# Kernel optimization log

Hardware: AMD Instinct MI355X
Metric: run time of the kernel (lower is better)

## Reference

```python
import jax, jax.numpy as jnp
import numpy as np

D_EMB = 1024
D_MODEL = 1024
NUM_ROLES = 4
ROLE_DIM = 64
ROPE_BASE = 10000.0
LN_EPS = 1e-5


def _rope_cos_sin(positions):
    # positions: [B, S] float -> cos, sin: [B, S, D_MODEL//2]
    inv_freq = 1.0 / (ROPE_BASE ** (jnp.arange(0, D_MODEL, 2, dtype=jnp.float32) / D_MODEL))
    freqs = positions[..., None] * inv_freq  # [B,S,d/2]
    return jnp.cos(freqs), jnp.sin(freqs)


def _apply_rotary(x, cos, sin):
    d = x.shape[-1] // 2
    x1, x2 = x[..., :d], x[..., d:]
    return jnp.concatenate([x1 * cos - x2 * sin, x1 * sin + x2 * cos], axis=-1)


def _layernorm(x, g, b):
    mu = jnp.mean(x, axis=-1, keepdims=True)
    var = jnp.var(x, axis=-1, keepdims=True)
    return (x - mu) * jax.lax.rsqrt(var + LN_EPS) * g + b


def setup_inputs() -> dict:
    key = jax.random.key(0)
    ks = jax.random.split(key, 16)
    B, S, M = 16, 4096, 200
    inp = {}
    inp["x_ctx"] = jax.random.normal(ks[0], (B, M, D_EMB), dtype=jnp.float32)
    inp["x_suf"] = jax.random.normal(ks[1], (B, S, D_EMB), dtype=jnp.float32)
    inp["pos_ctx"] = jax.random.randint(ks[2], (B, M), 0, 8192, dtype=jnp.int32)
    inp["pos_suf"] = jnp.sort(jax.random.randint(ks[3], (B, S), 0, 8192, dtype=jnp.int32), axis=-1)
    inp["role_ctx"] = jax.random.randint(ks[4], (B, M), 0, NUM_ROLES, dtype=jnp.int32)
    inp["role_tgt"] = jax.random.randint(ks[5], (B,), 0, NUM_ROLES, dtype=jnp.int32)
    inp["mask_ctx"] = jax.random.randint(ks[6], (B, M), 0, 2, dtype=jnp.int32)
    inp["mask_suf"] = jax.random.randint(ks[7], (B, S), 0, 2, dtype=jnp.int32)
    # parameters
    inp["ln_g"] = jnp.ones((D_EMB,), jnp.float32)
    inp["ln_b"] = jnp.zeros((D_EMB,), jnp.float32)
    inp["hist_role_emb"] = jax.random.normal(ks[8], (NUM_ROLES, ROLE_DIM), dtype=jnp.float32)
    inp["tgt_role_emb"] = jax.random.normal(ks[9], (NUM_ROLES, ROLE_DIM), dtype=jnp.float32)
    inp["start_state"] = jax.random.normal(ks[10], (D_EMB + ROLE_DIM,), dtype=jnp.float32) * 0.02
    inp["wq"] = jax.random.normal(ks[11], (D_MODEL, D_EMB + 2 * ROLE_DIM), dtype=jnp.float32) * 0.02
    inp["wk"] = jax.random.normal(ks[12], (D_MODEL, D_EMB), dtype=jnp.float32) * 0.02
    inp["u_w1"] = jax.random.normal(ks[13], (D_MODEL, D_EMB), dtype=jnp.float32) * 0.02
    inp["u_b1"] = jnp.zeros((D_MODEL,), jnp.float32)
    inp["u_w2"] = jax.random.normal(ks[14], (NUM_ROLES, D_MODEL), dtype=jnp.float32) * 0.02
    inp["u_b2"] = jnp.zeros((NUM_ROLES,), jnp.float32)
    return inp


def reference(x_ctx, x_suf, pos_ctx, pos_suf, role_ctx, role_tgt, mask_ctx, mask_suf,
              ln_g, ln_b, hist_role_emb, tgt_role_emb, start_state,
              wq, wk, u_w1, u_b1, u_w2, u_b2):
    B, S, _ = x_suf.shape
    scale = 1.0 / jnp.sqrt(jnp.asarray(D_MODEL, jnp.float32))

    # ---- history summary: last valid token's features + its role embedding ----
    lengths = jnp.sum(mask_ctx.astype(jnp.int32), axis=1)          # [B]
    last_idx = jnp.clip(lengths - 1, 0, None)                       # [B]
    last_x = jnp.take_along_axis(x_ctx, last_idx[:, None, None], axis=1)[:, 0]  # [B, d_emb]
    last_role = jnp.take_along_axis(role_ctx, last_idx[:, None], axis=1)[:, 0]  # [B]
    cand = jnp.concatenate([last_x, hist_role_emb[last_role]], axis=-1)  # [B, d_emb+role_dim]
    summary = jnp.where((lengths > 0)[:, None], cand, start_state[None, :])

    # ---- query / keys ----
    q_in = jnp.concatenate([summary, tgt_role_emb[role_tgt]], axis=-1)  # [B, d_emb+2*role_dim]
    x_s = _layernorm(x_suf, ln_g, ln_b)                                 # [B, S, d_emb]

    anchor = pos_suf[:, :1].astype(jnp.float32) - 1.0                   # [B, 1]
    q_cos, q_sin = _rope_cos_sin(anchor)                                # [B, 1, d/2]
    k_cos, k_sin = _rope_cos_sin(pos_suf.astype(jnp.float32))           # [B, S, d/2]

    q = (q_in @ wq.T)[:, None, :]                                       # [B, 1, d_model]
    k = jnp.einsum('bse,de->bsd', x_s, wk)                              # [B, S, d_model]
    q = _apply_rotary(q, q_cos, q_sin)
    k = _apply_rotary(k, k_cos, k_sin)

    logits = jnp.einsum('bd,bsd->bs', q[:, 0], k) * scale               # [B, S]

    # ---- unary logits, gathered at target role ----
    h = jax.nn.gelu(jnp.einsum('bse,de->bsd', x_s, u_w1) + u_b1, approximate=False)
    unary_all = jnp.einsum('bsd,rd->bsr', h, u_w2) + u_b2               # [B, S, num_roles]
    unary = jnp.take_along_axis(unary_all, role_tgt[:, None, None].astype(jnp.int32), axis=-1)[..., 0]
    logits = logits + unary

    logits = jnp.where(mask_suf == 0, -jnp.inf, logits)
    return logits, jnp.argmax(logits, axis=-1)
```

## Files before the change

### kernel.cpp

```cpp
#include <hip/hip_runtime.h>
#include <math.h>

#define B_SZ 16
#define S_LEN 4096
#define M_CTX 200
#define DE 1024
#define NTOK (B_SZ * S_LEN)

#define MASK_SENTINEL -3.0e38f

typedef __attribute__((ext_vector_type(8))) short short8v;
typedef __attribute__((ext_vector_type(4))) float f32x4;

__device__ __forceinline__ unsigned short f2bf(float f) {
  unsigned x = __float_as_uint(f);
  unsigned r = x + 0x7fffu + ((x >> 16) & 1u);
  return (unsigned short)(r >> 16);
}
__device__ __forceinline__ float bf2f(unsigned short u) {
  return __uint_as_float(((unsigned)u) << 16);
}
__device__ __forceinline__ void gload16(const unsigned short* g, short* l) {
  __builtin_amdgcn_global_load_lds(
      (const __attribute__((address_space(1))) unsigned int*)g,
      (__attribute__((address_space(3))) unsigned int*)l, 16, 0, 0);
}

__global__ __launch_bounds__(256) void invf_kernel(float* __restrict__ invf_g) {
  int i = blockIdx.x * 256 + threadIdx.x;
  invf_g[i] = 1.0f / powf(10000.0f, (float)(2 * i) * (1.0f / 1024.0f));
}

__global__ __launch_bounds__(256) void prep_qin_kernel(
    const float* __restrict__ x_ctx, const int* __restrict__ role_ctx,
    const int* __restrict__ role_tgt, const int* __restrict__ mask_ctx,
    const float* __restrict__ hist_role_emb, const float* __restrict__ tgt_role_emb,
    const float* __restrict__ start_state, float* __restrict__ qin_ws)
{
  int b = blockIdx.x;
  int tid = threadIdx.x;
  __shared__ int sh[3];
  if (tid == 0) {
    int len = 0;
    for (int m = 0; m < M_CTX; ++m) len += (mask_ctx[b * M_CTX + m] != 0) ? 1 : 0;
    int li = len - 1; if (li < 0) li = 0;
    sh[0] = len; sh[1] = li; sh[2] = role_ctx[b * M_CTX + li];
  }
  __syncthreads();
  int len = sh[0], li = sh[1], lrole = sh[2];
  int rt = role_tgt[b];
  for (int e = tid; e < 1152; e += 256) {
    float v;
    if (e < 1024)      v = (len > 0) ? x_ctx[((size_t)b * M_CTX + li) * DE + e] : start_state[e];
    else if (e < 1088) v = (len > 0) ? hist_role_emb[lrole * 64 + (e - 1024)] : start_state[e];
    else               v = tgt_role_emb[rt * 64 + (e - 1088)];
    qin_ws[b * 1152 + e] = v;
  }
}

__global__ __launch_bounds__(256) void matvec_q_kernel(
    const float* __restrict__ qin_ws, const float* __restrict__ wq,
    float* __restrict__ qv_ws)
{
  int dblk = blockIdx.x, b = blockIdx.y;
  int tid = threadIdx.x, lane = tid & 63, w = tid >> 6;
  __shared__ float q[1152];
  for (int i = tid; i < 1152; i += 256) q[i] = qin_ws[b * 1152 + i];
  __syncthreads();
  #pragma unroll 4
  for (int i = 0; i < 16; ++i) {
    int d = dblk * 64 + w * 16 + i;
    const float* wr = wq + (size_t)d * 1152;
    float s = 0.f;
    #pragma unroll
    for (int j = 0; j < 18; ++j) s += q[j * 64 + lane] * wr[j * 64 + lane];
    #pragma unroll
    for (int off = 32; off; off >>= 1) s += __shfl_down(s, off);
    if (lane == 0) qv_ws[b * 1024 + d] = s;
  }
}

__global__ __launch_bounds__(256) void rot_q_kernel(
    const float* __restrict__ qv_ws, const float* __restrict__ invf_g,
    const int* __restrict__ pos_suf, float* __restrict__ q_rot)
{
  int b = blockIdx.x;
  int tid = threadIdx.x;
  float anchor = (float)pos_suf[(size_t)b * S_LEN] - 1.0f;
  const float scl = 1.0f / 32.0f;
  for (int i = tid; i < 512; i += 256) {
    float sn, cs;
    sincosf(anchor * invf_g[i], &sn, &cs);
    float q1 = qv_ws[b * 1024 + i], q2 = qv_ws[b * 1024 + i + 512];
    q_rot[b * 1024 + i]       = (q1 * cs - q2 * sn) * scl;
    q_rot[b * 1024 + i + 512] = (q1 * sn + q2 * cs) * scl;
  }
}

__global__ __launch_bounds__(256) void split_A_kernel(
    const float* __restrict__ x_suf, const float* __restrict__ ln_g,
    const float* __restrict__ ln_b,
    unsigned short* __restrict__ Ah, unsigned short* __restrict__ Al)
{
  int wave = threadIdx.x >> 6;
  int lane = threadIdx.x & 63;
  size_t t = (size_t)blockIdx.x * 4 + wave;
  const float4* xp = (const float4*)(x_suf + t * DE);
  float4 v[4];
  float s = 0.f, sq = 0.f;
  #pragma unroll
  for (int i = 0; i < 4; ++i) {
    v[i] = xp[lane + 64 * i];
    s  += v[i].x + v[i].y + v[i].z + v[i].w;
    sq += v[i].x * v[i].x + v[i].y * v[i].y + v[i].z * v[i].z + v[i].w * v[i].w;
  }
  #pragma unroll
  for (int off = 32; off; off >>= 1) {
    s  += __shfl_down(s, off);
    sq += __shfl_down(sq, off);
  }
  s = __shfl(s, 0); sq = __shfl(sq, 0);
  float m = s * (1.0f / 1024.0f);
  float rs = rsqrtf(sq * (1.0f / 1024.0f) - m * m + 1e-5f);
  #pragma unroll
  for (int i = 0; i < 4; ++i) {
    int e0 = (lane + 64 * i) * 4;
    float4 gv = *(const float4*)&ln_g[e0];
    float4 bv = *(const float4*)&ln_b[e0];
    float a0 = (v[i].x - m) * rs * gv.x + bv.x;
    float a1 = (v[i].y - m) * rs * gv.y + bv.y;
    float a2 = (v[i].z - m) * rs * gv.z + bv.z;
    float a3 = (v[i].w - m) * rs * gv.w + bv.w;
    ushort4 hi, lo;
    hi.x = f2bf(a0); lo.x = f2bf(a0 - bf2f(hi.x));
    hi.y = f2bf(a1); lo.y = f2bf(a1 - bf2f(hi.y));
    hi.z = f2bf(a2); lo.z = f2bf(a2 - bf2f(hi.z));
    hi.w = f2bf(a3); lo.w = f2bf(a3 - bf2f(hi.w));
    *(ushort4*)&Ah[t * DE + e0] = hi;
    *(ushort4*)&Al[t * DE + e0] = lo;
  }
}

__global__ __launch_bounds__(256) void split_B_kernel(
    const float* __restrict__ wk, const float* __restrict__ u_w1,
    unsigned short* __restrict__ Bh, unsigned short* __restrict__ Bl)
{
  size_t i4 = (size_t)blockIdx.x * 256 + threadIdx.x;
  size_t e0 = i4 * 4;
  size_t row = e0 >> 10;
  size_t off = e0 & 1023;
  const float* src = (row < 1024) ? (wk + row * 1024 + off)
                                  : (u_w1 + (row - 1024) * 1024 + off);
  float4 v = *(const float4*)src;
  ushort4 hi, lo;
  hi.x = f2bf(v.x); lo.x = f2bf(v.x - bf2f(hi.x));
  hi.y = f2bf(v.y); lo.y = f2bf(v.y - bf2f(hi.y));
  hi.z = f2bf(v.z); lo.z = f2bf(v.z - bf2f(hi.z));
  hi.w = f2bf(v.w); lo.w = f2bf(v.w - bf2f(hi.w));
  *(ushort4*)&Bh[e0] = hi;
  *(ushort4*)&Bl[e0] = lo;
}

__global__ __launch_bounds__(256, 2) void mfma_gemm_kernel(
    const unsigned short* __restrict__ Ah, const unsigned short* __restrict__ Al,
    const unsigned short* __restrict__ Bh, const unsigned short* __restrict__ Bl,
    unsigned short* __restrict__ kb, unsigned short* __restrict__ hb)
{
  __shared__ __align__(16) short lAh[128 * 32];
  __shared__ __align__(16) short lAl[128 * 32];
  __shared__ __align__(16) short lBh[128 * 32];
  __shared__ __align__(16) short lBl[128 * 32];

  int lin = blockIdx.y * 16 + blockIdx.x;
  int swz = (lin & 7) * 1024 + (lin >> 3);
  int nt = swz & 15;
  size_t gt0 = (size_t)(swz >> 4) * 128;
  int tid = threadIdx.x;
  int lane = tid & 63;
  int wid = tid >> 6;
  int wr = wid >> 1, wc = wid & 1;
  size_t n0 = (size_t)nt * 128;

  const unsigned short* gsrc; short* ldst; size_t rbase;
  if (wid == 0)      { gsrc = Ah; ldst = lAh; rbase = gt0; }
  else if (wid == 1) { gsrc = Al; ldst = lAl; rbase = gt0; }
  else if (wid == 2) { gsrc = Bh; ldst = lBh; rbase = n0; }
  else               { gsrc = Bl; ldst = lBl; rbase = n0; }

  f32x4 acc[4][4];
  #pragma unroll
  for (int i = 0; i < 4; ++i)
    #pragma unroll
    for (int j = 0; j < 4; ++j) acc[i][j] = (f32x4)0.f;

  for (int kk = 0; kk < 1024; kk += 32) {
    #pragma unroll
    for (int it = 0; it < 8; ++it) {
      int row = it * 16 + (lane >> 2);
      int g = (lane & 3) ^ ((row >> 1) & 3);
      gload16(gsrc + (rbase + row) * 1024 + kk + g * 8, ldst + it * 512);
    }
    __syncthreads();

    short8v a_h[4], a_l[4], b_h[4], b_l[4];
    #pragma unroll
    for (int f = 0; f < 4; ++f) {
      int r = wr * 64 + f * 16 + (lane & 15);
      int idx = r * 32 + (((lane >> 4) ^ ((r >> 1) & 3)) << 3);
      a_h[f] = *(const short8v*)&lAh[idx];
      a_l[f] = *(const short8v*)&lAl[idx];
      int c = wc * 64 + f * 16 + (lane & 15);
      int idxb = c * 32 + (((lane >> 4) ^ ((c >> 1) & 3)) << 3);
      b_h[f] = *(const short8v*)&lBh[idxb];
      b_l[f] = *(const short8v*)&lBl[idxb];
    }

    #define MFMA_(ACC, A, B) \
      asm volatile("v_mfma_f32_16x16x32_bf16 %0, %1, %2, %0" : "+v"(ACC) : "v"(A), "v"(B))
    #pragma unroll
    for (int i = 0; i < 4; ++i)
      #pragma unroll
      for (int j = 0; j < 4; ++j) MFMA_(acc[i][j], a_h[i], b_h[j]);
    #pragma unroll
    for (int i = 0; i < 4; ++i)
      #pragma unroll
      for (int j = 0; j < 4; ++j) MFMA_(acc[i][j], a_h[i], b_l[j]);
    #pragma unroll
    for (int i = 0; i < 4; ++i)
      #pragma unroll
      for (int j = 0; j < 4; ++j) MFMA_(acc[i][j], a_l[i], b_h[j]);
    #undef MFMA_
    __syncthreads();
  }

  asm volatile("s_nop 7\n\ts_nop 7\n\ts_nop 7");

  unsigned short* outb = (nt < 8) ? kb : hb;
  size_t ncol0 = (nt < 8) ? n0 : n0 - 1024;
  #pragma unroll
  for (int fi = 0; fi < 4; ++fi)
    #pragma unroll
    for (int fj = 0; fj < 4; ++fj) {
      size_t col = ncol0 + wc * 64 + fj * 16 + (lane & 15);
      #pragma unroll
      for (int r = 0; r < 4; ++r) {
        size_t t = gt0 + wr * 64 + fi * 16 + (lane >> 4) * 4 + r;
        outb[t * 1024 + col] = f2bf(acc[fi][fj][r]);
      }
    }
}

__global__ __launch_bounds__(256) void ep_kernel(
    const unsigned short* __restrict__ kb, const unsigned short* __restrict__ hb,
    const float* __restrict__ q_rot, const float* __restrict__ invf_g,
    const int* __restrict__ pos_suf, const int* __restrict__ role_tgt,
    const float* __restrict__ u_b1, const float* __restrict__ u_w2,
    const float* __restrict__ u_b2, const int* __restrict__ mask_suf,
    float* __restrict__ out)
{
  __shared__ float sInv[512];
  for (int i = threadIdx.x; i < 512; i += 256) sInv[i] = invf_g[i];
  __syncthreads();

  int wave = threadIdx.x >> 6;
  int lane = threadIdx.x & 63;
  size_t t = (size_t)blockIdx.x * 4 + wave;
  int b = (int)(t >> 12);
  int role = role_tgt[b];
  float pos = (float)pos_suf[t];
  float s = 0.f;

  {
    int c0 = lane * 8;
    short8v k1 = *(const short8v*)&kb[t * 1024 + c0];
    short8v k2 = *(const short8v*)&kb[t * 1024 + 512 + c0];
    float4 q1a = *(const float4*)&q_rot[b * 1024 + c0];
    float4 q1b = *(const float4*)&q_rot[b * 1024 + c0 + 4];
    float4 q2a = *(const float4*)&q_rot[b * 1024 + 512 + c0];
    float4 q2b = *(const float4*)&q_rot[b * 1024 + 512 + c0 + 4];
    float q1v[8] = {q1a.x, q1a.y, q1a.z, q1a.w, q1b.x, q1b.y, q1b.z, q1b.w};
    float q2v[8] = {q2a.x, q2a.y, q2a.z, q2a.w, q2b.x, q2b.y, q2b.z, q2b.w};
    #pragma unroll
    for (int j = 0; j < 8; ++j) {
      float sn, cs;
      sincosf(pos * sInv[c0 + j], &sn, &cs);
      s += bf2f((unsigned short)k1[j]) * (q1v[j] * cs + q2v[j] * sn)
         + bf2f((unsigned short)k2[j]) * (q2v[j] * cs - q1v[j] * sn);
    }
  }
  {
    int c0 = lane * 16;
    short8v h1 = *(const short8v*)&hb[t * 1024 + c0];
    short8v h2 = *(const short8v*)&hb[t * 1024 + c0 + 8];
    #pragma unroll
    for (int half = 0; half < 2; ++half) {
      short8v hv = half ? h2 : h1;
      int cc = c0 + half * 8;
      float4 b1a = *(const float4*)&u_b1[cc];
      float4 b1b = *(const float4*)&u_b1[cc + 4];
      float4 w2a = *(const float4*)&u_w2[role * 1024 + cc];
      float4 w2b = *(const float4*)&u_w2[role * 1024 + cc + 4];
      float b1v[8] = {b1a.x, b1a.y, b1a.z, b1a.w, b1b.x, b1b.y, b1b.z, b1b.w};
      float w2v[8] = {w2a.x, w2a.y, w2a.z, w2a.w, w2b.x, w2b.y, w2b.z, w2b.w};
      #pragma unroll
      for (int j = 0; j < 8; ++j) {
        float pre = bf2f((unsigned short)hv[j]) + b1v[j];
        float g = pre * 0.5f * (1.0f + erff(pre * 0.70710678118f));
        s += g * w2v[j];
      }
    }
  }
  #pragma unroll
  for (int off = 32; off; off >>= 1) s += __shfl_down(s, off);
  if (lane == 0) {
    float v = s + u_b2[role];
    if (mask_suf[t] == 0) v = MASK_SENTINEL;
    out[t] = v;
  }
}

__global__ __launch_bounds__(256) void argmax_kernel(
    const float* __restrict__ logits, float* __restrict__ out)
{
  int b = blockIdx.x;
  int tid = threadIdx.x;
  float bestv = -INFINITY;
  int besti = 0x7fffffff;
  for (int s = tid; s < S_LEN; s += 256) {
    float v = logits[(size_t)b * S_LEN + s];
    if (v > bestv || (v == bestv && s < besti)) { bestv = v; besti = s; }
  }
  __shared__ float sv[256];
  __shared__ int si[256];
  sv[tid] = bestv; si[tid] = besti;
  __syncthreads();
  for (int off = 128; off; off >>= 1) {
    if (tid < off) {
      float ov = sv[tid + off]; int oi = si[tid + off];
      if (ov > sv[tid] || (ov == sv[tid] && oi < si[tid])) { sv[tid] = ov; si[tid] = oi; }
    }
    __syncthreads();
  }
  if (tid == 0) out[(size_t)B_SZ * S_LEN + b] = (float)si[0];
}

__global__ __launch_bounds__(256) void ln_stats_kernel(
    const float* __restrict__ x_suf, float* __restrict__ mu, float* __restrict__ rstd)
{
  int wave = threadIdx.x >> 6;
  int lane = threadIdx.x & 63;
  size_t t = (size_t)blockIdx.x * 4 + wave;
  const float4* xp = (const float4*)(x_suf + t * DE);
  float s = 0.f, sq = 0.f;
  #pragma unroll
  for (int i = 0; i < 4; ++i) {
    float4 v = xp[lane + 64 * i];
    s  += v.x + v.y + v.z + v.w;
    sq += v.x * v.x + v.y * v.y + v.z * v.z + v.w * v.w;
  }
  #pragma unroll
  for (int off = 32; off; off >>= 1) {
    s  += __shfl_down(s, off);
    sq += __shfl_down(sq, off);
  }
  if (lane == 0) {
    float m = s * (1.0f / 1024.0f);
    float var = sq * (1.0f / 1024.0f) - m * m;
    mu[t] = m;
    rstd[t] = rsqrtf(var + 1e-5f);
  }
}

#define BM 128
#define BN 128
#define BKF 32
#define LDP 132

__global__ __launch_bounds__(256) void main_gemm_kernel(
    const float* __restrict__ x_suf, const float* __restrict__ wk,
    const float* __restrict__ u_w1, const float* __restrict__ ln_g,
    const float* __restrict__ ln_b, const float* __restrict__ mu,
    const float* __restrict__ rstd, const float* __restrict__ q_rot,
    const int* __restrict__ pos_suf, const int* __restrict__ role_tgt,
    const float* __restrict__ u_b1, const float* __restrict__ u_w2,
    float* __restrict__ accb)
{
  __shared__ float As[BKF][LDP];
  __shared__ float Bs[BKF][LDP];
  __shared__ float sInvf[512];

  int nt = blockIdx.x;
  size_t tt = blockIdx.y;
  int tid = threadIdx.x;
  size_t gt0 = tt * BM;
  int b = (int)(gt0 >> 12);

  for (int i = tid; i < 512; i += 256)
    sInvf[i] = 1.0f / powf(10000.0f, (float)(2 * i) * (1.0f / 1024.0f));

  int lr = tid >> 3;
  int lc = (tid & 7) * 4;
  float lmu[4], lrs[4];
  #pragma unroll
  for (int r = 0; r < 4; ++r) {
    lmu[r] = mu[gt0 + lr + 32 * r];
    lrs[r] = rstd[gt0 + lr + 32 * r];
  }
  const float* Wb = (nt < 8) ? wk : u_w1;
  int rowoff = (nt < 8) ? nt * BN : nt * BN - 1024;

  float acc[8][8];
  #pragma unroll
  for (int i = 0; i < 8; ++i)
    #pragma unroll
    for (int j = 0; j < 8; ++j) acc[i][j] = 0.f;

  int tx = tid & 15, ty = tid >> 4;

  for (int kk = 0; kk < 1024; kk += BKF) {
    float4 gv = *(const float4*)&ln_g[kk + lc];
    float4 bv = *(const float4*)&ln_b[kk + lc];
    #pragma unroll
    for (int r = 0; r < 4; ++r) {
      int row = lr + 32 * r;
      float4 xv = *(const float4*)&x_suf[(gt0 + row) * (size_t)DE + kk + lc];
      float m = lmu[r], rs = lrs[r];
      As[lc + 0][row] = (xv.x - m) * rs * gv.x + bv.x;
      As[lc + 1][row] = (xv.y - m) * rs * gv.y + bv.y;
      As[lc + 2][row] = (xv.z - m) * rs * gv.z + bv.z;
      As[lc + 3][row] = (xv.w - m) * rs * gv.w + bv.w;
      float4 wv = *(const float4*)&Wb[(size_t)(rowoff + row) * 1024 + kk + lc];
      Bs[lc + 0][row] = wv.x;
      Bs[lc + 1][row] = wv.y;
      Bs[lc + 2][row] = wv.z;
      Bs[lc + 3][row] = wv.w;
    }
    __syncthreads();
    #pragma unroll 8
    for (int k = 0; k < BKF; ++k) {
      float a[8], bb[8];
      *(float4*)&a[0]  = *(const float4*)&As[k][ty * 8];
      *(float4*)&a[4]  = *(const float4*)&As[k][ty * 8 + 4];
      *(float4*)&bb[0] = *(const float4*)&Bs[k][tx * 8];
      *(float4*)&bb[4] = *(const float4*)&Bs[k][tx * 8 + 4];
      #pragma unroll
      for (int i = 0; i < 8; ++i)
        #pragma unroll
        for (int j = 0; j < 8; ++j)
          acc[i][j] += a[i] * bb[j];
    }
    __syncthreads();
  }

  int role = role_tgt[b];
  float part[8];
  int cb = nt * BN + tx * 8;
  if (nt < 8) {
    #pragma unroll
    for (int i = 0; i < 8; ++i) {
      size_t t = gt0 + ty * 8 + i;
      float pos = (float)pos_suf[t];
      float p = 0.f;
      #pragma unroll
      for (int j = 0; j < 8; ++j) {
        int c = cb + j;
        int ii = (c < 512) ? c : (c - 512);
        float sn, cs;
        sincosf(pos * sInvf[ii], &sn, &cs);
        float q1 = q_rot[b * 1024 + ii];
        float q2 = q_rot[b * 1024 + ii + 512];
        float qe = (c < 512) ? (q1 * cs + q2 * sn) : (q2 * cs - q1 * sn);
        p += acc[i][j] * qe;
      }
      part[i] = p;
    }
  } else {
    #pragma unroll
    for (int i = 0; i < 8; ++i) {
      float p = 0.f;
      #pragma unroll
      for (int j = 0; j < 8; ++j) {
        int c = cb - 1024 + j;
        float pre = acc[i][j] + u_b1[c];
        float h = pre * 0.5f * (1.0f + erff(pre * 0.70710678118f));
        p += h * u_w2[role * 1024 + c];
      }
      part[i] = p;
    }
  }
  #pragma unroll
  for (int off = 8; off >= 1; off >>= 1) {
    #pragma unroll
    for (int i = 0; i < 8; ++i) part[i] += __shfl_down(part[i], off, 16);
  }
  if (tx == 0) {
    #pragma unroll
    for (int i = 0; i < 8; ++i) atomicAdd(&accb[gt0 + ty * 8 + i], part[i]);
  }
}

__global__ __launch_bounds__(256) void finalize_kernel(
    const float* __restrict__ accb, const int* __restrict__ mask_suf,
    const int* __restrict__ role_tgt, const float* __restrict__ u_b2,
    float* __restrict__ out)
{
  int b = blockIdx.x;
  int tid = threadIdx.x;
  float ub = u_b2[role_tgt[b]];
  float bestv = -INFINITY;
  int besti = 0x7fffffff;
  for (int s = tid; s < S_LEN; s += 256) {
    float v = accb[(size_t)b * S_LEN + s] + ub;
    if (mask_suf[(size_t)b * S_LEN + s] == 0) v = MASK_SENTINEL;
    out[(size_t)b * S_LEN + s] = v;
    if (v > bestv || (v == bestv && s < besti)) { bestv = v; besti = s; }
  }
  __shared__ float sv[256];
  __shared__ int si[256];
  sv[tid] = bestv; si[tid] = besti;
  __syncthreads();
  for (int off = 128; off; off >>= 1) {
    if (tid < off) {
      float ov = sv[tid + off]; int oi = si[tid + off];
      if (ov > sv[tid] || (ov == sv[tid] && oi < si[tid])) { sv[tid] = ov; si[tid] = oi; }
    }
    __syncthreads();
  }
  if (tid == 0) out[(size_t)B_SZ * S_LEN + b] = (float)si[0];
}

extern "C" void kernel_launch(void* const* d_in, const int* in_sizes, int n_in,
                              void* d_out, int out_size, void* d_ws, size_t ws_size,
                              hipStream_t stream)
{
  const float* x_ctx         = (const float*)d_in[0];
  const float* x_suf         = (const float*)d_in[1];
  const int*   pos_suf       = (const int*)d_in[3];
  const int*   role_ctx      = (const int*)d_in[4];
  const int*   role_tgt      = (const int*)d_in[5];
  const int*   mask_ctx      = (const int*)d_in[6];
  const int*   mask_suf      = (const int*)d_in[7];
  const float* ln_g          = (const float*)d_in[8];
  const float* ln_b          = (const float*)d_in[9];
  const float* hist_role_emb = (const float*)d_in[10];
  const float* tgt_role_emb  = (const float*)d_in[11];
  const float* start_state   = (const float*)d_in[12];
  const float* wq            = (const float*)d_in[13];
  const float* wk            = (const float*)d_in[14];
  const float* u_w1          = (const float*)d_in[15];
  const float* u_b1          = (const float*)d_in[16];
  const float* u_w2          = (const float*)d_in[17];
  const float* u_b2          = (const float*)d_in[18];
  float* out = (float*)d_out;
  char* ws = (char*)d_ws;

  const size_t OFF_QROT = 0;
  const size_t OFF_INVF = 65536;
  const size_t OFF_QIN  = OFF_INVF + 4096;
  const size_t OFF_QV   = OFF_QIN + 81920;
  const size_t OFF_BH   = 1 << 20;
  const size_t OFF_BL   = OFF_BH + 4194304;
  const size_t OFF_AH   = OFF_BL + 4194304;
  const size_t OFF_AL   = OFF_AH + 134217728;
  const size_t OFF_KB   = OFF_AL + 134217728;
  const size_t OFF_HB   = OFF_KB + 134217728;
  const size_t NEEDED   = OFF_HB + 134217728;

  if (ws_size >= NEEDED) {
    float* q_rot = (float*)(ws + OFF_QROT);
    float* invf_g = (float*)(ws + OFF_INVF);
    float* qin_ws = (float*)(ws + OFF_QIN);
    float* qv_ws  = (float*)(ws + OFF_QV);
    unsigned short* Bh = (unsigned short*)(ws + OFF_BH);
    unsigned short* Bl = (unsigned short*)(ws + OFF_BL);
    unsigned short* Ah = (unsigned short*)(ws + OFF_AH);
    unsigned short* Al = (unsigned short*)(ws + OFF_AL);
    unsigned short* kb = (unsigned short*)(ws + OFF_KB);
    unsigned short* hb = (unsigned short*)(ws + OFF_HB);

    invf_kernel<<<2, 256, 0, stream>>>(invf_g);
    prep_qin_kernel<<<B_SZ, 256, 0, stream>>>(
        x_ctx, role_ctx, role_tgt, mask_ctx,
        hist_role_emb, tgt_role_emb, start_state, qin_ws);
    matvec_q_kernel<<<dim3(16, B_SZ), 256, 0, stream>>>(qin_ws, wq, qv_ws);
    rot_q_kernel<<<B_SZ, 256, 0, stream>>>(qv_ws, invf_g, pos_suf, q_rot);
    split_B_kernel<<<2048, 256, 0, stream>>>(wk, u_w1, Bh, Bl);
    split_A_kernel<<<NTOK / 4, 256, 0, stream>>>(x_suf, ln_g, ln_b, Ah, Al);
    dim3 gg(16, NTOK / 128);
    mfma_gemm_kernel<<<gg, 256, 0, stream>>>(Ah, Al, Bh, Bl, kb, hb);
    ep_kernel<<<NTOK / 4, 256, 0, stream>>>(
        kb, hb, q_rot, invf_g, pos_suf, role_tgt, u_b1, u_w2, u_b2, mask_suf, out);
    argmax_kernel<<<B_SZ, 256, 0, stream>>>(out, out);
  } else {
    float* q_rot = (float*)ws;
    float* mu    = (float*)(ws + (64 << 10));
    float* rstd  = (float*)(ws + (64 << 10) + (256 << 10));
    float* accb  = (float*)(ws + (64 << 10) + (512 << 10));

    hipMemsetAsync(accb, 0, NTOK * sizeof(float), stream);
    prep_qin_kernel<<<B_SZ, 256, 0, stream>>>(
        x_ctx, role_ctx, role_tgt, mask_ctx,
        hist_role_emb, tgt_role_emb, start_state, q_rot);
    matvec_q_kernel<<<dim3(16, B_SZ), 256, 0, stream>>>(q_rot, wq, rstd);
    rot_q_kernel<<<B_SZ, 256, 0, stream>>>(rstd, mu, pos_suf, q_rot);
    ln_stats_kernel<<<NTOK / 4, 256, 0, stream>>>(x_suf, mu, rstd);
    dim3 g3(16, NTOK / BM);
    main_gemm_kernel<<<g3, 256, 0, stream>>>(
        x_suf, wk, u_w1, ln_g, ln_b, mu, rstd, q_rot,
        pos_suf, role_tgt, u_b1, u_w2, accb);
    finalize_kernel<<<B_SZ, 256, 0, stream>>>(accb, mask_suf, role_tgt, u_b2, out);
  }
}
```

Baseline: 1.288 ms.

## Fuse RoPE/GELU epilogue into MFMA GEMM with atomic row reduction

The GEMM epilogue now applies the rotary dot product with q, or GELU with the u_w2 projection, directly on the accumulators. It reduces across the 16 lanes of a row and atomically adds per-token partial sums into a float buffer. The two 128MB bf16 intermediates (kb, hb) and the separate epilogue kernel are removed, and argmax is merged with the mask/bias finalize step. The block swizzle is dropped for a plain grid mapping, which may hurt L2 reuse. The fused epilogue also adds sincos/erf work and atomics inside the GEMM, and atomic ordering makes the sums nondeterministic.

```diff
diff --git a/kernel.cpp b/kernel.cpp
--- a/kernel.cpp
+++ b/kernel.cpp
@@ -161,25 +161,47 @@
   *(ushort4*)&Bl[e0] = lo;
 }
 
-__global__ __launch_bounds__(256, 2) void mfma_gemm_kernel(
+__global__ __launch_bounds__(256, 2) void mfma_gemm_fused_kernel(
     const unsigned short* __restrict__ Ah, const unsigned short* __restrict__ Al,
     const unsigned short* __restrict__ Bh, const unsigned short* __restrict__ Bl,
-    unsigned short* __restrict__ kb, unsigned short* __restrict__ hb)
+    const float* __restrict__ q_rot, const float* __restrict__ invf_g,
+    const int* __restrict__ pos_suf, const int* __restrict__ role_tgt,
+    const float* __restrict__ u_b1, const float* __restrict__ u_w2,
+    float* __restrict__ accb)
 {
   __shared__ __align__(16) short lAh[128 * 32];
   __shared__ __align__(16) short lAl[128 * 32];
   __shared__ __align__(16) short lBh[128 * 32];
   __shared__ __align__(16) short lBl[128 * 32];
-
-  int lin = blockIdx.y * 16 + blockIdx.x;
-  int swz = (lin & 7) * 1024 + (lin >> 3);
-  int nt = swz & 15;
-  size_t gt0 = (size_t)(swz >> 4) * 128;
+  __shared__ float sPos[128];
+  __shared__ float sC0[128];
+  __shared__ float sC1[128];
+  __shared__ float sC2[128];
+
+  int nt = blockIdx.x;
+  size_t gt0 = (size_t)blockIdx.y * 128;
+  int b = (int)(gt0 >> 12);
   int tid = threadIdx.x;
   int lane = tid & 63;
   int wid = tid >> 6;
   int wr = wid >> 1, wc = wid & 1;
   size_t n0 = (size_t)nt * 128;
+
+  if (tid < 128) {
+    int j = tid;
+    sPos[j] = (float)pos_suf[gt0 + j];
+    if (nt < 8) {
+      int c = nt * 128 + j;
+      int ii = c & 511;
+      sC0[j] = q_rot[b * 1024 + ii];
+      sC1[j] = q_rot[b * 1024 + ii + 512];
+      sC2[j] = invf_g[ii];
+    } else {
+      int cc = nt * 128 - 1024 + j;
+      sC0[j] = u_b1[cc];
+      sC1[j] = u_w2[role_tgt[b] * 1024 + cc];
+    }
+  }
 
   const unsigned short* gsrc; short* ldst; size_t rbase;
   if (wid == 0)      { gsrc = Ah; ldst = lAh; rbase = gt0; }
@@ -235,99 +257,76 @@
 
   asm volatile("s_nop 7\n\ts_nop 7\n\ts_nop 7");
 
-  unsigned short* outb = (nt < 8) ? kb : hb;
-  size_t ncol0 = (nt < 8) ? n0 : n0 - 1024;
+  float vsum[4][4];
+  if (nt < 8) {
+    bool lowhalf = (nt < 4);
+    #pragma unroll
+    for (int fi = 0; fi < 4; ++fi)
+      #pragma unroll
+      for (int r = 0; r < 4; ++r) {
+        int row = wr * 64 + fi * 16 + ((lane >> 4) << 2) + r;
+        float p = sPos[row];
+        float vs = 0.f;
+        #pragma unroll
+        for (int fj = 0; fj < 4; ++fj) {
+          int j = wc * 64 + fj * 16 + (lane & 15);
+          float sn, cs;
+          sincosf(p * sC2[j], &sn, &cs);
+          float qe = lowhalf ? (sC0[j] * cs + sC1[j] * sn)
+                             : (sC1[j] * cs - sC0[j] * sn);
+          vs += acc[fi][fj][r] * qe;
+        }
+        vsum[fi][r] = vs;
+      }
+  } else {
+    #pragma unroll
+    for (int fi = 0; fi < 4; ++fi)
+      #pragma unroll
+      for (int r = 0; r < 4; ++r) {
+        float vs = 0.f;
+        #pragma unroll
+        for (int fj = 0; fj < 4; ++fj) {
+          int j = wc * 64 + fj * 16 + (lane & 15);
+          float pre = acc[fi][fj][r] + sC0[j];
+          float g = pre * 0.5f * (1.0f + erff(pre * 0.70710678118f));
+          vs += g * sC1[j];
+        }
+        vsum[fi][r] = vs;
+      }
+  }
   #pragma unroll
   for (int fi = 0; fi < 4; ++fi)
     #pragma unroll
-    for (int fj = 0; fj < 4; ++fj) {
-      size_t col = ncol0 + wc * 64 + fj * 16 + (lane & 15);
+    for (int r = 0; r < 4; ++r) {
+      #pragma unroll
+      for (int off = 1; off < 16; off <<= 1)
+        vsum[fi][r] += __shfl_xor(vsum[fi][r], off, 16);
+    }
+  if ((lane & 15) == 0) {
+    #pragma unroll
+    for (int fi = 0; fi < 4; ++fi)
       #pragma unroll
       for (int r = 0; r < 4; ++r) {
-        size_t t = gt0 + wr * 64 + fi * 16 + (lane >> 4) * 4 + r;
-        outb[t * 1024 + col] = f2bf(acc[fi][fj][r]);
+        size_t t = gt0 + wr * 64 + fi * 16 + ((lane >> 4) << 2) + r;
+        atomicAdd(&accb[t], vsum[fi][r]);
       }
-    }
-}
-
-__global__ __launch_bounds__(256) void ep_kernel(
-    const unsigned short* __restrict__ kb, const unsigned short* __restrict__ hb,
-    const float* __restrict__ q_rot, const float* __restrict__ invf_g,
-    const int* __restrict__ pos_suf, const int* __restrict__ role_tgt,
-    const float* __restrict__ u_b1, const float* __restrict__ u_w2,
-    const float* __restrict__ u_b2, const int* __restrict__ mask_suf,
+  }
+}
+
+__global__ __launch_bounds__(256) void finalize_kernel(
+    const float* __restrict__ accb, const int* __restrict__ mask_suf,
+    const int* __restrict__ role_tgt, const float* __restrict__ u_b2,
     float* __restrict__ out)
-{
-  __shared__ float sInv[512];
-  for (int i = threadIdx.x; i < 512; i += 256) sInv[i] = invf_g[i];
-  __syncthreads();
-
-  int wave = threadIdx.x >> 6;
-  int lane = threadIdx.x & 63;
-  size_t t = (size_t)blockIdx.x * 4 + wave;
-  int b = (int)(t >> 12);
-  int role = role_tgt[b];
-  float pos = (float)pos_suf[t];
-  float s = 0.f;
-
-  {
-    int c0 = lane * 8;
-    short8v k1 = *(const short8v*)&kb[t * 1024 + c0];
-    short8v k2 = *(const short8v*)&kb[t * 1024 + 512 + c0];
-    float4 q1a = *(const float4*)&q_rot[b * 1024 + c0];
-    float4 q1b = *(const float4*)&q_rot[b * 1024 + c0 + 4];
-    float4 q2a = *(const float4*)&q_rot[b * 1024 + 512 + c0];
-    float4 q2b = *(const float4*)&q_rot[b * 1024 + 512 + c0 + 4];
-    float q1v[8] = {q1a.x, q1a.y, q1a.z, q1a.w, q1b.x, q1b.y, q1b.z, q1b.w};
-    float q2v[8] = {q2a.x, q2a.y, q2a.z, q2a.w, q2b.x, q2b.y, q2b.z, q2b.w};
-    #pragma unroll
-    for (int j = 0; j < 8; ++j) {
-      float sn, cs;
-      sincosf(pos * sInv[c0 + j], &sn, &cs);
-      s += bf2f((unsigned short)k1[j]) * (q1v[j] * cs + q2v[j] * sn)
-         + bf2f((unsigned short)k2[j]) * (q2v[j] * cs - q1v[j] * sn);
-    }
-  }
-  {
-    int c0 = lane * 16;
-    short8v h1 = *(const short8v*)&hb[t * 1024 + c0];
-    short8v h2 = *(const short8v*)&hb[t * 1024 + c0 + 8];
-    #pragma unroll
-    for (int half = 0; half < 2; ++half) {
-      short8v hv = half ? h2 : h1;
-      int cc = c0 + half * 8;
-      float4 b1a = *(const float4*)&u_b1[cc];
-      float4 b1b = *(const float4*)&u_b1[cc + 4];
-      float4 w2a = *(const float4*)&u_w2[role * 1024 + cc];
-      float4 w2b = *(const float4*)&u_w2[role * 1024 + cc + 4];
-      float b1v[8] = {b1a.x, b1a.y, b1a.z, b1a.w, b1b.x, b1b.y, b1b.z, b1b.w};
-      float w2v[8] = {w2a.x, w2a.y, w2a.z, w2a.w, w2b.x, w2b.y, w2b.z, w2b.w};
-      #pragma unroll
-      for (int j = 0; j < 8; ++j) {
-        float pre = bf2f((unsigned short)hv[j]) + b1v[j];
-        float g = pre * 0.5f * (1.0f + erff(pre * 0.70710678118f));
-        s += g * w2v[j];
-      }
-    }
-  }
-  #pragma unroll
-  for (int off = 32; off; off >>= 1) s += __shfl_down(s, off);
-  if (lane == 0) {
-    float v = s + u_b2[role];
-    if (mask_suf[t] == 0) v = MASK_SENTINEL;
-    out[t] = v;
-  }
-}
-
-__global__ __launch_bounds__(256) void argmax_kernel(
-    const float* __restrict__ logits, float* __restrict__ out)
 {
   int b = blockIdx.x;
   int tid = threadIdx.x;
+  float ub = u_b2[role_tgt[b]];
   float bestv = -INFINITY;
   int besti = 0x7fffffff;
   for (int s = tid; s < S_LEN; s += 256) {
-    float v = logits[(size_t)b * S_LEN + s];
+    float v = accb[(size_t)b * S_LEN + s] + ub;
+    if (mask_suf[(size_t)b * S_LEN + s] == 0) v = MASK_SENTINEL;
+    out[(size_t)b * S_LEN + s] = v;
     if (v > bestv || (v == bestv && s < besti)) { bestv = v; besti = s; }
   }
   __shared__ float sv[256];
@@ -497,36 +496,6 @@
     #pragma unroll
     for (int i = 0; i < 8; ++i) atomicAdd(&accb[gt0 + ty * 8 + i], part[i]);
   }
-}
-
-__global__ __launch_bounds__(256) void finalize_kernel(
-    const float* __restrict__ accb, const int* __restrict__ mask_suf,
-    const int* __restrict__ role_tgt, const float* __restrict__ u_b2,
-    float* __restrict__ out)
-{
-  int b = blockIdx.x;
-  int tid = threadIdx.x;
-  float ub = u_b2[role_tgt[b]];
-  float bestv = -INFINITY;
-  int besti = 0x7fffffff;
-  for (int s = tid; s < S_LEN; s += 256) {
-    float v = accb[(size_t)b * S_LEN + s] + ub;
-    if (mask_suf[(size_t)b * S_LEN + s] == 0) v = MASK_SENTINEL;
-    out[(size_t)b * S_LEN + s] = v;
-    if (v > bestv || (v == bestv && s < besti)) { bestv = v; besti = s; }
-  }
-  __shared__ float sv[256];
-  __shared__ int si[256];
-  sv[tid] = bestv; si[tid] = besti;
-  __syncthreads();
-  for (int off = 128; off; off >>= 1) {
-    if (tid < off) {
-      float ov = sv[tid + off]; int oi = si[tid + off];
-      if (ov > sv[tid] || (ov == sv[tid] && oi < si[tid])) { sv[tid] = ov; si[tid] = oi; }
-    }
-    __syncthreads();
-  }
-  if (tid == 0) out[(size_t)B_SZ * S_LEN + b] = (float)si[0];
 }
 
 extern "C" void kernel_launch(void* const* d_in, const int* in_sizes, int n_in,
@@ -558,26 +527,25 @@
   const size_t OFF_INVF = 65536;
   const size_t OFF_QIN  = OFF_INVF + 4096;
   const size_t OFF_QV   = OFF_QIN + 81920;
+  const size_t OFF_ACCB = OFF_QV + 65536;
   const size_t OFF_BH   = 1 << 20;
   const size_t OFF_BL   = OFF_BH + 4194304;
   const size_t OFF_AH   = OFF_BL + 4194304;
   const size_t OFF_AL   = OFF_AH + 134217728;
-  const size_t OFF_KB   = OFF_AL + 134217728;
-  const size_t OFF_HB   = OFF_KB + 134217728;
-  const size_t NEEDED   = OFF_HB + 134217728;
+  const size_t NEEDED   = OFF_AL + 134217728;
 
   if (ws_size >= NEEDED) {
-    float* q_rot = (float*)(ws + OFF_QROT);
+    float* q_rot  = (float*)(ws + OFF_QROT);
     float* invf_g = (float*)(ws + OFF_INVF);
     float* qin_ws = (float*)(ws + OFF_QIN);
     float* qv_ws  = (float*)(ws + OFF_QV);
+    float* accb   = (float*)(ws + OFF_ACCB);
     unsigned short* Bh = (unsigned short*)(ws + OFF_BH);
     unsigned short* Bl = (unsigned short*)(ws + OFF_BL);
     unsigned short* Ah = (unsigned short*)(ws + OFF_AH);
     unsigned short* Al = (unsigned short*)(ws + OFF_AL);
-    unsigned short* kb = (unsigned short*)(ws + OFF_KB);
-    unsigned short* hb = (unsigned short*)(ws + OFF_HB);
-
+
+    hipMemsetAsync(accb, 0, NTOK * sizeof(float), stream);
     invf_kernel<<<2, 256, 0, stream>>>(invf_g);
     prep_qin_kernel<<<B_SZ, 256, 0, stream>>>(
         x_ctx, role_ctx, role_tgt, mask_ctx,
@@ -587,22 +555,25 @@
     split_B_kernel<<<2048, 256, 0, stream>>>(wk, u_w1, Bh, Bl);
     split_A_kernel<<<NTOK / 4, 256, 0, stream>>>(x_suf, ln_g, ln_b, Ah, Al);
     dim3 gg(16, NTOK / 128);
-    mfma_gemm_kernel<<<gg, 256, 0, stream>>>(Ah, Al, Bh, Bl, kb, hb);
-    ep_kernel<<<NTOK / 4, 256, 0, stream>>>(
-        kb, hb, q_rot, invf_g, pos_suf, role_tgt, u_b1, u_w2, u_b2, mask_suf, out);
-    argmax_kernel<<<B_SZ, 256, 0, stream>>>(out, out);
+    mfma_gemm_fused_kernel<<<gg, 256, 0, stream>>>(
+        Ah, Al, Bh, Bl, q_rot, invf_g, pos_suf, role_tgt, u_b1, u_w2, accb);
+    finalize_kernel<<<B_SZ, 256, 0, stream>>>(accb, mask_suf, role_tgt, u_b2, out);
   } else {
-    float* q_rot = (float*)ws;
-    float* mu    = (float*)(ws + (64 << 10));
-    float* rstd  = (float*)(ws + (64 << 10) + (256 << 10));
-    float* accb  = (float*)(ws + (64 << 10) + (512 << 10));
+    float* q_rot  = (float*)ws;
+    float* mu     = (float*)(ws + (64 << 10));
+    float* rstd   = (float*)(ws + (320 << 10));
+    float* accb   = (float*)(ws + (576 << 10));
+    float* qin_ws = (float*)(ws + (832 << 10));
+    float* qv_ws  = (float*)(ws + (912 << 10));
+    float* invf_g = (float*)(ws + (976 << 10));
 
     hipMemsetAsync(accb, 0, NTOK * sizeof(float), stream);
+    invf_kernel<<<2, 256, 0, stream>>>(invf_g);
     prep_qin_kernel<<<B_SZ, 256, 0, stream>>>(
         x_ctx, role_ctx, role_tgt, mask_ctx,
-        hist_role_emb, tgt_role_emb, start_state, q_rot);
-    matvec_q_kernel<<<dim3(16, B_SZ), 256, 0, stream>>>(q_rot, wq, rstd);
-    rot_q_kernel<<<B_SZ, 256, 0, stream>>>(rstd, mu, pos_suf, q_rot);
+        hist_role_emb, tgt_role_emb, start_state, qin_ws);
+    matvec_q_kernel<<<dim3(16, B_SZ), 256, 0, stream>>>(qin_ws, wq, qv_ws);
+    rot_q_kernel<<<B_SZ, 256, 0, stream>>>(qv_ws, invf_g, pos_suf, q_rot);
     ln_stats_kernel<<<NTOK / 4, 256, 0, stream>>>(x_suf, mu, rstd);
     dim3 g3(16, NTOK / BM);
     main_gemm_kernel<<<g3, 256, 0, stream>>>(
```

New measurement: 4.291 ms. +233.2%, slower.

## Precompute RoPE cos/sin lookup table and simplify epilogue and GEMM tile mapping

Applied to the files above, without the earlier changes.

Adds a kernel that builds per-position cos/sin tables for all 8192 possible positions, so the epilogue reads them instead of calling sincosf per element. The epilogue loads are reorganised to strided per-lane scalar accesses, and the GEMM drops its block-index swizzle in favour of a direct mapping. The fallback path's workspace layout is also fixed so it stops aliasing buffers. The table costs 32 MB of writes plus gather reads per token, and removing the swizzle may hurt L2 reuse in the GEMM.

```diff
diff --git a/kernel.cpp b/kernel.cpp
--- a/kernel.cpp
+++ b/kernel.cpp
@@ -6,6 +6,7 @@
 #define M_CTX 200
 #define DE 1024
 #define NTOK (B_SZ * S_LEN)
+#define POS_MAX 8192
 
 #define MASK_SENTINEL -3.0e38f
 
@@ -29,6 +30,20 @@
 __global__ __launch_bounds__(256) void invf_kernel(float* __restrict__ invf_g) {
   int i = blockIdx.x * 256 + threadIdx.x;
   invf_g[i] = 1.0f / powf(10000.0f, (float)(2 * i) * (1.0f / 1024.0f));
+}
+
+__global__ __launch_bounds__(256) void lut_kernel(
+    const float* __restrict__ invf_g,
+    float* __restrict__ lutc, float* __restrict__ luts)
+{
+  int p = blockIdx.x;
+  float fp = (float)p;
+  for (int c = threadIdx.x; c < 512; c += 256) {
+    float sn, cs;
+    sincosf(fp * invf_g[c], &sn, &cs);
+    lutc[(size_t)p * 512 + c] = cs;
+    luts[(size_t)p * 512 + c] = sn;
+  }
 }
 
 __global__ __launch_bounds__(256) void prep_qin_kernel(
@@ -171,10 +186,8 @@
   __shared__ __align__(16) short lBh[128 * 32];
   __shared__ __align__(16) short lBl[128 * 32];
 
-  int lin = blockIdx.y * 16 + blockIdx.x;
-  int swz = (lin & 7) * 1024 + (lin >> 3);
-  int nt = swz & 15;
-  size_t gt0 = (size_t)(swz >> 4) * 128;
+  int nt = blockIdx.x;
+  size_t gt0 = (size_t)blockIdx.y * 128;
   int tid = threadIdx.x;
   int lane = tid & 63;
   int wid = tid >> 6;
@@ -252,63 +265,41 @@
 
 __global__ __launch_bounds__(256) void ep_kernel(
     const unsigned short* __restrict__ kb, const unsigned short* __restrict__ hb,
-    const float* __restrict__ q_rot, const float* __restrict__ invf_g,
-    const int* __restrict__ pos_suf, const int* __restrict__ role_tgt,
-    const float* __restrict__ u_b1, const float* __restrict__ u_w2,
-    const float* __restrict__ u_b2, const int* __restrict__ mask_suf,
-    float* __restrict__ out)
-{
-  __shared__ float sInv[512];
-  for (int i = threadIdx.x; i < 512; i += 256) sInv[i] = invf_g[i];
-  __syncthreads();
-
+    const float* __restrict__ q_rot, const float* __restrict__ lutc,
+    const float* __restrict__ luts, const int* __restrict__ pos_suf,
+    const int* __restrict__ role_tgt, const float* __restrict__ u_b1,
+    const float* __restrict__ u_w2, const float* __restrict__ u_b2,
+    const int* __restrict__ mask_suf, float* __restrict__ out)
+{
   int wave = threadIdx.x >> 6;
   int lane = threadIdx.x & 63;
   size_t t = (size_t)blockIdx.x * 4 + wave;
   int b = (int)(t >> 12);
   int role = role_tgt[b];
-  float pos = (float)pos_suf[t];
+  size_t lbase = (size_t)pos_suf[t] * 512;
+  const unsigned short* kp = kb + t * 1024;
+  const unsigned short* hp = hb + t * 1024;
+  const float* lc = lutc + lbase;
+  const float* ls = luts + lbase;
+  const float* qr = q_rot + b * 1024;
+  const float* w2 = u_w2 + role * 1024;
   float s = 0.f;
 
-  {
-    int c0 = lane * 8;
-    short8v k1 = *(const short8v*)&kb[t * 1024 + c0];
-    short8v k2 = *(const short8v*)&kb[t * 1024 + 512 + c0];
-    float4 q1a = *(const float4*)&q_rot[b * 1024 + c0];
-    float4 q1b = *(const float4*)&q_rot[b * 1024 + c0 + 4];
-    float4 q2a = *(const float4*)&q_rot[b * 1024 + 512 + c0];
-    float4 q2b = *(const float4*)&q_rot[b * 1024 + 512 + c0 + 4];
-    float q1v[8] = {q1a.x, q1a.y, q1a.z, q1a.w, q1b.x, q1b.y, q1b.z, q1b.w};
-    float q2v[8] = {q2a.x, q2a.y, q2a.z, q2a.w, q2b.x, q2b.y, q2b.z, q2b.w};
-    #pragma unroll
-    for (int j = 0; j < 8; ++j) {
-      float sn, cs;
-      sincosf(pos * sInv[c0 + j], &sn, &cs);
-      s += bf2f((unsigned short)k1[j]) * (q1v[j] * cs + q2v[j] * sn)
-         + bf2f((unsigned short)k2[j]) * (q2v[j] * cs - q1v[j] * sn);
-    }
-  }
-  {
-    int c0 = lane * 16;
-    short8v h1 = *(const short8v*)&hb[t * 1024 + c0];
-    short8v h2 = *(const short8v*)&hb[t * 1024 + c0 + 8];
-    #pragma unroll
-    for (int half = 0; half < 2; ++half) {
-      short8v hv = half ? h2 : h1;
-      int cc = c0 + half * 8;
-      float4 b1a = *(const float4*)&u_b1[cc];
-      float4 b1b = *(const float4*)&u_b1[cc + 4];
-      float4 w2a = *(const float4*)&u_w2[role * 1024 + cc];
-      float4 w2b = *(const float4*)&u_w2[role * 1024 + cc + 4];
-      float b1v[8] = {b1a.x, b1a.y, b1a.z, b1a.w, b1b.x, b1b.y, b1b.z, b1b.w};
-      float w2v[8] = {w2a.x, w2a.y, w2a.z, w2a.w, w2b.x, w2b.y, w2b.z, w2b.w};
-      #pragma unroll
-      for (int j = 0; j < 8; ++j) {
-        float pre = bf2f((unsigned short)hv[j]) + b1v[j];
-        float g = pre * 0.5f * (1.0f + erff(pre * 0.70710678118f));
-        s += g * w2v[j];
-      }
-    }
+  #pragma unroll
+  for (int j = 0; j < 8; ++j) {
+    int c = lane + 64 * j;
+    float k1 = bf2f(kp[c]);
+    float k2 = bf2f(kp[c + 512]);
+    float q1 = qr[c], q2 = qr[c + 512];
+    float cs = lc[c], sn = ls[c];
+    s += k1 * (q1 * cs + q2 * sn) + k2 * (q2 * cs - q1 * sn);
+  }
+  #pragma unroll
+  for (int j = 0; j < 16; ++j) {
+    int c = lane + 64 * j;
+    float pre = bf2f(hp[c]) + u_b1[c];
+    float g = pre * 0.5f * (1.0f + erff(pre * 0.70710678118f));
+    s += g * w2[c];
   }
   #pragma unroll
   for (int off = 32; off; off >>= 1) s += __shfl_down(s, off);
@@ -556,21 +547,25 @@
 
   const size_t OFF_QROT = 0;
   const size_t OFF_INVF = 65536;
-  const size_t OFF_QIN  = OFF_INVF + 4096;
-  const size_t OFF_QV   = OFF_QIN + 81920;
+  const size_t OFF_QIN  = 69632;
+  const size_t OFF_QV   = 151552;
   const size_t OFF_BH   = 1 << 20;
   const size_t OFF_BL   = OFF_BH + 4194304;
-  const size_t OFF_AH   = OFF_BL + 4194304;
+  const size_t OFF_LUTC = OFF_BL + 4194304;
+  const size_t OFF_LUTS = OFF_LUTC + 16777216;
+  const size_t OFF_AH   = OFF_LUTS + 16777216;
   const size_t OFF_AL   = OFF_AH + 134217728;
   const size_t OFF_KB   = OFF_AL + 134217728;
   const size_t OFF_HB   = OFF_KB + 134217728;
   const size_t NEEDED   = OFF_HB + 134217728;
 
   if (ws_size >= NEEDED) {
-    float* q_rot = (float*)(ws + OFF_QROT);
+    float* q_rot  = (float*)(ws + OFF_QROT);
     float* invf_g = (float*)(ws + OFF_INVF);
     float* qin_ws = (float*)(ws + OFF_QIN);
     float* qv_ws  = (float*)(ws + OFF_QV);
+    float* lutc   = (float*)(ws + OFF_LUTC);
+    float* luts   = (float*)(ws + OFF_LUTS);
     unsigned short* Bh = (unsigned short*)(ws + OFF_BH);
     unsigned short* Bl = (unsigned short*)(ws + OFF_BL);
     unsigned short* Ah = (unsigned short*)(ws + OFF_AH);
@@ -579,6 +574,7 @@
     unsigned short* hb = (unsigned short*)(ws + OFF_HB);
 
     invf_kernel<<<2, 256, 0, stream>>>(invf_g);
+    lut_kernel<<<POS_MAX, 256, 0, stream>>>(invf_g, lutc, luts);
     prep_qin_kernel<<<B_SZ, 256, 0, stream>>>(
         x_ctx, role_ctx, role_tgt, mask_ctx,
         hist_role_emb, tgt_role_emb, start_state, qin_ws);
@@ -589,20 +585,25 @@
     dim3 gg(16, NTOK / 128);
     mfma_gemm_kernel<<<gg, 256, 0, stream>>>(Ah, Al, Bh, Bl, kb, hb);
     ep_kernel<<<NTOK / 4, 256, 0, stream>>>(
-        kb, hb, q_rot, invf_g, pos_suf, role_tgt, u_b1, u_w2, u_b2, mask_suf, out);
+        kb, hb, q_rot, lutc, luts, pos_suf, role_tgt, u_b1, u_w2, u_b2,
+        mask_suf, out);
     argmax_kernel<<<B_SZ, 256, 0, stream>>>(out, out);
   } else {
-    float* q_rot = (float*)ws;
-    float* mu    = (float*)(ws + (64 << 10));
-    float* rstd  = (float*)(ws + (64 << 10) + (256 << 10));
-    float* accb  = (float*)(ws + (64 << 10) + (512 << 10));
+    float* q_rot  = (float*)ws;
+    float* mu     = (float*)(ws + (64 << 10));
+    float* rstd   = (float*)(ws + (320 << 10));
+    float* accb   = (float*)(ws + (576 << 10));
+    float* qin_ws = (float*)(ws + (832 << 10));
+    float* qv_ws  = (float*)(ws + (912 << 10));
+    float* invf_g = (float*)(ws + (976 << 10));
 
     hipMemsetAsync(accb, 0, NTOK * sizeof(float), stream);
+    invf_kernel<<<2, 256, 0, stream>>>(invf_g);
     prep_qin_kernel<<<B_SZ, 256, 0, stream>>>(
         x_ctx, role_ctx, role_tgt, mask_ctx,
-        hist_role_emb, tgt_role_emb, start_state, q_rot);
-    matvec_q_kernel<<<dim3(16, B_SZ), 256, 0, stream>>>(q_rot, wq, rstd);
-    rot_q_kernel<<<B_SZ, 256, 0, stream>>>(rstd, mu, pos_suf, q_rot);
+        hist_role_emb, tgt_role_emb, start_state, qin_ws);
+    matvec_q_kernel<<<dim3(16, B_SZ), 256, 0, stream>>>(qin_ws, wq, qv_ws);
+    rot_q_kernel<<<B_SZ, 256, 0, stream>>>(qv_ws, invf_g, pos_suf, q_rot);
     ln_stats_kernel<<<NTOK / 4, 256, 0, stream>>>(x_suf, mu, rstd);
     dim3 g3(16, NTOK / BM);
     main_gemm_kernel<<<g3, 256, 0, stream>>>(
```

Result: slower. 1.351 ms (+4.9%).
